# Kernel optimization log

Hardware: AMD Instinct MI355X
Metric: run time of the kernel (lower is better)

The kernel has to match this reference:

```python
import jax, jax.numpy as jnp
import numpy as np

N = 50000      # nodes
E = 600000     # edges
G = 256        # graphs in batch
HID = 128      # gcn hidden = gcn in = gcn out
EDIM = 16      # edge feature dim
EH = 64        # edge mlp hidden
NL = 4         # gcn layers
MIN_ = 200     # mol feature dim
MH = 256       # mlp hidden
MOUT = 128     # mlp out
PH = 512       # predictor hidden
PIN = HID + MOUT


def setup_inputs() -> dict:
    key = jax.random.key(0)
    ks = jax.random.split(key, 32)
    f = lambda k, s: jax.random.normal(k, s, dtype=jnp.float32)
    p = lambda k, s: 0.05 * jax.random.normal(k, s, dtype=jnp.float32)
    return {
        "x": f(ks[0], (N, HID)),
        "edge_index": jax.random.randint(ks[1], (2, E), 0, N),
        "edge_attr": f(ks[2], (E, EDIM)),
        "batch_index": jnp.sort(jax.random.randint(ks[3], (N,), 0, G)),
        "mol_features": f(ks[4], (G, MIN_)),
        # PDNConv params (stacked over NL layers)
        "conv_lin_W": p(ks[5], (NL, HID, HID)),
        "conv_mW1": p(ks[6], (NL, EDIM, EH)),
        "conv_mb1": p(ks[7], (NL, EH)),
        "conv_mW2": p(ks[8], (NL, EH)),
        "conv_mb2": p(ks[9], (NL,)),
        "conv_bias": p(ks[10], (NL, HID)),
        # dense Linear after each conv
        "gcn_W": p(ks[11], (NL, HID, HID)),
        "gcn_b": p(ks[12], (NL, HID)),
        # mol-feature MLP (n_mlp_layers=3 -> 4 linears)
        "mlp_W0": p(ks[13], (MIN_, MH)), "mlp_b0": p(ks[14], (MH,)),
        "mlp_W1": p(ks[15], (MH, MH)),   "mlp_b1": p(ks[16], (MH,)),
        "mlp_W2": p(ks[17], (MH, MH)),   "mlp_b2": p(ks[18], (MH,)),
        "mlp_W3": p(ks[19], (MH, MOUT)), "mlp_b3": p(ks[20], (MOUT,)),
        # predictor
        "pred_W0": p(ks[21], (PIN, PH)), "pred_b0": p(ks[22], (PH,)),
        "pred_W1": p(ks[23], (PH, PH)),  "pred_b1": p(ks[24], (PH,)),
        "out_W": p(ks[25], (PH, 1)),     "out_b": p(ks[26], (1,)),
    }


def _pdn_conv(h, row, col, edge_attr, lin_W, mW1, mb1, mW2, mb2, bias):
    # edge MLP -> sigmoid gate (PyG PDNConv)
    w = jax.nn.sigmoid(jnp.maximum(edge_attr @ mW1 + mb1, 0.0) @ mW2 + mb2)  # [E]
    # gcn_norm with self loops (fill weight 1.0)
    loop = jnp.arange(N)
    r = jnp.concatenate([row, loop])
    c = jnp.concatenate([col, loop])
    w_all = jnp.concatenate([w, jnp.ones((N,), h.dtype)])
    deg = jax.ops.segment_sum(w_all, c, num_segments=N)
    dinv = jnp.where(deg > 0, jax.lax.rsqrt(deg), 0.0)
    norm = dinv[r] * w_all * dinv[c]                                          # [E+N]
    hl = h @ lin_W                                                            # [N,HID]
    out = jax.ops.segment_sum(norm[:, None] * hl[r], c, num_segments=N)
    return out + bias


def reference(x, edge_index, edge_attr, batch_index, mol_features,
              conv_lin_W, conv_mW1, conv_mb1, conv_mW2, conv_mb2, conv_bias,
              gcn_W, gcn_b,
              mlp_W0, mlp_b0, mlp_W1, mlp_b1, mlp_W2, mlp_b2, mlp_W3, mlp_b3,
              pred_W0, pred_b0, pred_W1, pred_b1, out_W, out_b):
    row, col = edge_index[0], edge_index[1]
    relu = lambda v: jnp.maximum(v, 0.0)

    # GCN stack: PDNConv -> relu(Linear), x NL
    h1 = x
    for i in range(NL):
        h1 = _pdn_conv(h1, row, col, edge_attr, conv_lin_W[i], conv_mW1[i],
                       conv_mb1[i], conv_mW2[i], conv_mb2[i], conv_bias[i])
        h1 = relu(h1 @ gcn_W[i] + gcn_b[i])
    # global mean pool over graphs
    sums = jax.ops.segment_sum(h1, batch_index, num_segments=G)
    cnts = jax.ops.segment_sum(jnp.ones((N,), h1.dtype), batch_index, num_segments=G)
    h1 = sums / jnp.maximum(cnts, 1.0)[:, None]                               # [G,HID]

    # molecular-feature MLP
    h2 = relu(mol_features @ mlp_W0 + mlp_b0)
    h2 = relu(h2 @ mlp_W1 + mlp_b1)
    h2 = relu(h2 @ mlp_W2 + mlp_b2)
    h2 = relu(h2 @ mlp_W3 + mlp_b3)                                           # [G,MOUT]

    h = jnp.concatenate([h1, h2], axis=1)                                     # [G,PIN]
    h = relu(h @ pred_W0 + pred_b0)
    h = relu(h @ pred_W1 + pred_b1)
    return h @ out_W + out_b                                                  # [G,1]
```

## Files before the change

### kernel.cpp

```cpp
#include <hip/hip_runtime.h>
#include <hip/hip_bf16.h>


#define NN 50000
#define EE 600000
#define GG 256
#define HID 128
#define EDIM 16
#define EHID 64
#define NL 4
#define MIN_F 200
#define MH 256
#define MOUT 128
#define PH 512
#define PIN 256
#define SCAN_B 196
#define PCH 8

typedef __hip_bfloat16 bf16;
typedef __attribute__((ext_vector_type(8))) short bf16x8;
typedef __attribute__((ext_vector_type(4))) float f32x4;

__device__ __forceinline__ float bfl(unsigned u) { return __uint_as_float(u << 16); }
__device__ __forceinline__ float bfh(unsigned u) { return __uint_as_float(u & 0xffff0000u); }
__device__ __forceinline__ float b2f(bf16 x) { return __bfloat162float(x); }
__device__ __forceinline__ float ldf(const void* p, long i, bool bf) {
  return bf ? __bfloat162float(((const bf16*)p)[i]) : ((const float*)p)[i];
}
__device__ __forceinline__ unsigned short f2bf_bits(float v) {
  bf16 h = __float2bfloat16(v);
  return *reinterpret_cast<unsigned short*>(&h);
}

__global__ void probe_kernel(const unsigned short* __restrict__ xs, int* flag) {
  if (threadIdx.x == 0 && blockIdx.x == 0) {
    int sane = 0;
    for (int i = 0; i < 128; i++) {
      unsigned e = (xs[i] >> 7) & 0xFF;
      if (e >= 96 && e <= 159) sane++;
    }
    *flag = (sane >= 112) ? 1 : 0;
  }
}

__global__ __launch_bounds__(256) void cvt_to_bf16(const void* __restrict__ in,
                                                   unsigned short* __restrict__ outp,
                                                   int n8, const int* __restrict__ flag) {
  bool bf = *flag != 0;
  int i = blockIdx.x * 256 + threadIdx.x;
  if (i >= n8) return;
  if (bf) {
    reinterpret_cast<uint4*>(outp)[i] = reinterpret_cast<const uint4*>(in)[i];
  } else {
    const float4* p = reinterpret_cast<const float4*>(in) + (size_t)i * 2;
    float4 v0 = p[0], v1 = p[1];
    ushort4 a, b;
    a.x = f2bf_bits(v0.x); a.y = f2bf_bits(v0.y);
    a.z = f2bf_bits(v0.z); a.w = f2bf_bits(v0.w);
    b.x = f2bf_bits(v1.x); b.y = f2bf_bits(v1.y);
    b.z = f2bf_bits(v1.z); b.w = f2bf_bits(v1.w);
    reinterpret_cast<ushort4*>(outp)[i * 2] = a;
    reinterpret_cast<ushort4*>(outp)[i * 2 + 1] = b;
  }
}

__global__ __launch_bounds__(256) void cvt_molf(const void* __restrict__ in,
                                                float* __restrict__ outp,
                                                const int* __restrict__ flag) {
  bool bf = *flag != 0;
  int i = blockIdx.x * 256 + threadIdx.x;
  if (i >= GG * 50) return;
  int row = i / 50, c4 = (i % 50) * 4;
  float4 v;
  if (bf) {
    const unsigned short* p = (const unsigned short*)in + (size_t)row * MIN_F + c4;
    uint2 u = *reinterpret_cast<const uint2*>(p);
    v.x = bfl(u.x); v.y = bfh(u.x); v.z = bfl(u.y); v.w = bfh(u.y);
  } else {
    v = *reinterpret_cast<const float4*>((const float*)in + (size_t)row * MIN_F + c4);
  }
  *reinterpret_cast<float4*>(&outp[(size_t)row * 256 + c4]) = v;
}

__global__ __launch_bounds__(256) void prep_fused_w(const void* __restrict__ lin_W,
                                                    const void* __restrict__ gW,
                                                    unsigned short* __restrict__ Wt,
                                                    const int* __restrict__ flag) {
  bool bf = *flag != 0;
  int idx = blockIdx.x * 256 + threadIdx.x;
  if (idx >= 4 * 16384) return;
  int l = idx >> 14;
  int rem = idx & 16383;
  int n = rem >> 7, k = rem & 127;
  float s = 0.f;
  long lb = (long)l * 16384;
  for (int m = 0; m < 128; m++)
    s += ldf(lin_W, lb + (long)k * 128 + m, bf) * ldf(gW, lb + (long)m * 128 + n, bf);
  Wt[idx] = f2bf_bits(s);
}

__global__ __launch_bounds__(128) void prep_fused_b(const void* __restrict__ cbias,
                                                    const void* __restrict__ gW,
                                                    const void* __restrict__ gb,
                                                    float* __restrict__ bprime,
                                                    const int* __restrict__ flag) {
  bool bf = *flag != 0;
  int idx = blockIdx.x * 128 + threadIdx.x;
  if (idx >= NL * HID) return;
  int l = idx >> 7, n = idx & 127;
  float s = ldf(gb, idx, bf);
  long lb = (long)l * 16384;
  for (int k = 0; k < 128; k++)
    s += ldf(cbias, (long)l * 128 + k, bf) * ldf(gW, lb + (long)k * 128 + n, bf);
  bprime[idx] = s;
}

__global__ __launch_bounds__(256) void prep_edge_w(const void* __restrict__ mW1,
                                                   const void* __restrict__ mb1,
                                                   unsigned short* __restrict__ W1t,
                                                   const int* __restrict__ flag) {
  bool bf = *flag != 0;
  int idx = blockIdx.x * 256 + threadIdx.x;
  if (idx >= 256 * 32) return;
  int col = idx >> 5, k = idx & 31;
  float v = 0.f;
  if (k < EDIM) v = ldf(mW1, (long)(col >> 6) * (EDIM * EHID) + (long)k * EHID + (col & 63), bf);
  else if (k == EDIM) v = ldf(mb1, col, bf);
  W1t[idx] = f2bf_bits(v);
}

__global__ __launch_bounds__(256) void prep_tail(
    const void* __restrict__ mlpW0, const void* __restrict__ mlpW1,
    const void* __restrict__ mlpW2, const void* __restrict__ mlpW3,
    const void* __restrict__ predW0, const void* __restrict__ predW1,
    unsigned short* __restrict__ T, const int* __restrict__ flag) {
  bool bf = *flag != 0;
  int idx = blockIdx.x * 256 + threadIdx.x;
  const void* src; int N, Kp, Ksrc, off;
  if      (idx < 65536)  { src = mlpW0;  N = 256; Kp = 256; Ksrc = 200; off = 0; }
  else if (idx < 131072) { src = mlpW1;  N = 256; Kp = 256; Ksrc = 256; off = 65536; }
  else if (idx < 196608) { src = mlpW2;  N = 256; Kp = 256; Ksrc = 256; off = 131072; }
  else if (idx < 229376) { src = mlpW3;  N = 128; Kp = 256; Ksrc = 256; off = 196608; }
  else if (idx < 360448) { src = predW0; N = 512; Kp = 256; Ksrc = 256; off = 229376; }
  else if (idx < 622592) { src = predW1; N = 512; Kp = 512; Ksrc = 512; off = 360448; }
  else return;
  int rem = idx - off;
  int n = rem / Kp, k = rem % Kp;
  float v = (k < Ksrc) ? ldf(src, (long)k * N + n, bf) : 0.f;
  T[idx] = f2bf_bits(v);
}

__global__ __launch_bounds__(256) void count_kernel(const int* __restrict__ ei,
                                                    int* __restrict__ cnt) {
  int e = blockIdx.x * 256 + threadIdx.x;
  if (e >= EE) return;
  int c = ei[EE + e];
  c = min(max(c, 0), NN - 1);
  atomicAdd(&cnt[c], 1);
}

__global__ __launch_bounds__(256) void scan_phase1(const int* __restrict__ cnt,
                                                   int* __restrict__ bsum) {
  __shared__ int red[256];
  int tid = threadIdx.x;
  int i = blockIdx.x * 256 + tid;
  red[tid] = (i < NN) ? cnt[i] : 0;
  __syncthreads();
  for (int off = 128; off > 0; off >>= 1) {
    if (tid < off) red[tid] += red[tid + off];
    __syncthreads();
  }
  if (tid == 0) bsum[blockIdx.x] = red[0];
}

__global__ __launch_bounds__(256) void scan_phase2(int* __restrict__ bsum,
                                                   int* __restrict__ offs) {
  __shared__ int buf[256];
  int tid = threadIdx.x;
  int v = (tid < SCAN_B) ? bsum[tid] : 0;
  buf[tid] = v;
  __syncthreads();
  for (int off = 1; off < 256; off <<= 1) {
    int t = (tid >= off) ? buf[tid - off] : 0;
    __syncthreads();
    buf[tid] += t;
    __syncthreads();
  }
  if (tid < SCAN_B) bsum[tid] = buf[tid] - v;
  if (tid == 255) offs[NN] = buf[255];
}

__global__ __launch_bounds__(256) void scan_phase3(const int* __restrict__ cnt,
                                                   const int* __restrict__ bsum,
                                                   int* __restrict__ offs) {
  __shared__ int buf[256];
  int tid = threadIdx.x;
  int i = blockIdx.x * 256 + tid;
  int v = (i < NN) ? cnt[i] : 0;
  buf[tid] = v;
  __syncthreads();
  for (int off = 1; off < 256; off <<= 1) {
    int t = (tid >= off) ? buf[tid - off] : 0;
    __syncthreads();
    buf[tid] += t;
    __syncthreads();
  }
  if (i < NN) offs[i] = bsum[blockIdx.x] + buf[tid] - v;
}

__global__ __launch_bounds__(256) void fill_kernel(const int* __restrict__ ei,
                                                   const int* __restrict__ offs,
                                                   int* __restrict__ cursor,
                                                   int2* __restrict__ csr_se) {
  int e = blockIdx.x * 256 + threadIdx.x;
  if (e >= EE) return;
  int c = ei[EE + e];
  c = min(max(c, 0), NN - 1);
  int pos = offs[c] + atomicAdd(&cursor[c], 1);
  pos = min(max(pos, 0), EE - 1);
  csr_se[pos] = make_int2(ei[e], e);
}

__global__ __launch_bounds__(256) void edge_mlp_mfma(
    const void* __restrict__ eattr, const unsigned short* __restrict__ W1t,
    const void* __restrict__ mW2, const void* __restrict__ mb2,
    float* __restrict__ w_all4, const int* __restrict__ flag) {
  bool bf = *flag != 0;
  int tid = threadIdx.x;
  int wave = tid >> 6, lane = tid & 63;
  int l15 = lane & 15, quad = lane >> 4;

  bf16x8 bfrag[16];
#pragma unroll
  for (int t = 0; t < 16; t++)
    bfrag[t] = *reinterpret_cast<const bf16x8*>(&W1t[(t * 16 + l15) * 32 + quad * 8]);

  float w2v[16];
#pragma unroll
  for (int t = 0; t < 16; t++) w2v[t] = ldf(mW2, t * 16 + l15, bf);
  float b2v0 = ldf(mb2, 0, bf), b2v1 = ldf(mb2, 1, bf);
  float b2v2 = ldf(mb2, 2, bf), b2v3 = ldf(mb2, 3, bf);
  float b2 = b2v0;
  b2 = (l15 == 1) ? b2v1 : b2;
  b2 = (l15 == 2) ? b2v2 : b2;
  b2 = (l15 == 3) ? b2v3 : b2;
  bool o1 = (l15 & 1) != 0;
  bool o2 = (l15 & 2) != 0;

  int ebase = blockIdx.x * 512 + wave * 128;
#pragma unroll 1
  for (int f = 0; f < 8; f++) {
    int fbase = ebase + f * 16;
    if (fbase < EE) {
      long erow = fbase + l15;
      bf16x8 a = (bf16x8){0, 0, 0, 0, 0, 0, 0, 0};
      if (quad < 2) {
        if (bf) {
          uint4 v = *reinterpret_cast<const uint4*>((const bf16*)eattr + erow * EDIM + quad * 8);
          a = *reinterpret_cast<bf16x8*>(&v);
        } else {
          const float4* p =
              reinterpret_cast<const float4*>((const float*)eattr + erow * EDIM + quad * 8);
          float4 v0 = p[0], v1 = p[1];
          a[0] = (short)f2bf_bits(v0.x); a[1] = (short)f2bf_bits(v0.y);
          a[2] = (short)f2bf_bits(v0.z); a[3] = (short)f2bf_bits(v0.w);
          a[4] = (short)f2bf_bits(v1.x); a[5] = (short)f2bf_bits(v1.y);
          a[6] = (short)f2bf_bits(v1.z); a[7] = (short)f2bf_bits(v1.w);
        }
      }
      if (quad == 2) a[0] = (short)0x3F80;
      float s00 = 0.f, s01 = 0.f, s02 = 0.f, s03 = 0.f;
      float s10 = 0.f, s11 = 0.f, s12 = 0.f, s13 = 0.f;
      float s20 = 0.f, s21 = 0.f, s22 = 0.f, s23 = 0.f;
      float s30 = 0.f, s31 = 0.f, s32 = 0.f, s33 = 0.f;
#define DO_T(T, S0, S1, S2, S3)                                               \
  {                                                                           \
    f32x4 acc = __builtin_amdgcn_mfma_f32_16x16x32_bf16(                      \
        a, bfrag[T], (f32x4){0.f, 0.f, 0.f, 0.f}, 0, 0, 0);                   \
    S0 += fmaxf(acc.x, 0.f) * w2v[T];                                         \
    S1 += fmaxf(acc.y, 0.f) * w2v[T];                                         \
    S2 += fmaxf(acc.z, 0.f) * w2v[T];                                         \
    S3 += fmaxf(acc.w, 0.f) * w2v[T];                                         \
  }
      DO_T(0,  s00, s01, s02, s03) DO_T(1,  s00, s01, s02, s03)
      DO_T(2,  s00, s01, s02, s03) DO_T(3,  s00, s01, s02, s03)
      DO_T(4,  s10, s11, s12, s13) DO_T(5,  s10, s11, s12, s13)
      DO_T(6,  s10, s11, s12, s13) DO_T(7,  s10, s11, s12, s13)
      DO_T(8,  s20, s21, s22, s23) DO_T(9,  s20, s21, s22, s23)
      DO_T(10, s20, s21, s22, s23) DO_T(11, s20, s21, s22, s23)
      DO_T(12, s30, s31, s32, s33) DO_T(13, s30, s31, s32, s33)
      DO_T(14, s30, s31, s32, s33) DO_T(15, s30, s31, s32, s33)
#undef DO_T
#define RS_STEP1(AR, S0R, S1R) \
  float AR = (o1 ? S1R : S0R) + __shfl_xor(o1 ? S0R : S1R, 1);
      RS_STEP1(a0, s00, s10)
      RS_STEP1(a1, s01, s11)
      RS_STEP1(a2, s02, s12)
      RS_STEP1(a3, s03, s13)
      RS_STEP1(bb0, s20, s30)
      RS_STEP1(bb1, s21, s31)
      RS_STEP1(bb2, s22, s32)
      RS_STEP1(bb3, s23, s33)
#undef RS_STEP1
      float c0 = (o2 ? bb0 : a0) + __shfl_xor(o2 ? a0 : bb0, 2);
      float c1 = (o2 ? bb1 : a1) + __shfl_xor(o2 ? a1 : bb1, 2);
      float c2 = (o2 ? bb2 : a2) + __shfl_xor(o2 ? a2 : bb2, 2);
      float c3 = (o2 ? bb3 : a3) + __shfl_xor(o2 ? a3 : bb3, 2);
      c0 += __shfl_xor(c0, 4); c1 += __shfl_xor(c1, 4);
      c2 += __shfl_xor(c2, 4); c3 += __shfl_xor(c3, 4);
      c0 += __shfl_xor(c0, 8); c1 += __shfl_xor(c1, 8);
      c2 += __shfl_xor(c2, 8); c3 += __shfl_xor(c3, 8);
      if (l15 < NL) {
        float g0 = 1.f / (1.f + __expf(-(c0 + b2)));
        float g1 = 1.f / (1.f + __expf(-(c1 + b2)));
        float g2 = 1.f / (1.f + __expf(-(c2 + b2)));
        float g3 = 1.f / (1.f + __expf(-(c3 + b2)));
        w_all4[(size_t)(fbase + quad * 4 + 0) * 4 + l15] = g0;
        w_all4[(size_t)(fbase + quad * 4 + 1) * 4 + l15] = g1;
        w_all4[(size_t)(fbase + quad * 4 + 2) * 4 + l15] = g2;
        w_all4[(size_t)(fbase + quad * 4 + 3) * 4 + l15] = g3;
      }
    }
  }
}

__global__ __launch_bounds__(256) void csr_gather(const int2* __restrict__ csr_se,
                                                  const float* __restrict__ w_all4,
                                                  float* __restrict__ csr_val) {
  int k = blockIdx.x * 256 + threadIdx.x;
  if (k >= EE) return;
  int eid = csr_se[k].y;
  eid = min(max(eid, 0), EE - 1);
  float4 w = reinterpret_cast<const float4*>(w_all4)[eid];
  csr_val[k] = w.x;
  csr_val[(size_t)EE + k] = w.y;
  csr_val[2 * (size_t)EE + k] = w.z;
  csr_val[3 * (size_t)EE + k] = w.w;
}

__global__ __launch_bounds__(256) void deg_kernel(const int* __restrict__ offs,
                                                  const float* __restrict__ csr_val,
                                                  float* __restrict__ dinv4) {
  int n = blockIdx.x * 256 + threadIdx.x;
  if (n >= NN) return;
  int s = offs[n], e = offs[n + 1];
  float d0 = 1.f, d1 = 1.f, d2 = 1.f, d3 = 1.f;
  for (int k = s; k < e; k++) {
    d0 += csr_val[k];
    d1 += csr_val[EE + k];
    d2 += csr_val[2 * (size_t)EE + k];
    d3 += csr_val[3 * (size_t)EE + k];
  }
  float4 o;
  o.x = rsqrtf(d0); o.y = rsqrtf(d1); o.z = rsqrtf(d2); o.w = rsqrtf(d3);
  reinterpret_cast<float4*>(dinv4)[n] = o;
}

__global__ __launch_bounds__(256) void csr_scale_kernel(const int2* __restrict__ csr_se,
                                                        const float* __restrict__ dinv4,
                                                        float* __restrict__ csr_val) {
  int k = blockIdx.x * 256 + threadIdx.x;
  if (k >= EE) return;
  int s = csr_se[k].x;
  s = min(max(s, 0), NN - 1);
  float4 d = reinterpret_cast<const float4*>(dinv4)[s];
  csr_val[k] *= d.x;
  csr_val[(size_t)EE + k] *= d.y;
  csr_val[2 * (size_t)EE + k] *= d.z;
  csr_val[3 * (size_t)EE + k] *= d.w;
}

__global__ __launch_bounds__(256) void gemm_nodes_bf16(
    const unsigned short* __restrict__ A16, const unsigned short* __restrict__ Wt,
    const float* __restrict__ bias, unsigned short* __restrict__ out16,
    int relu) {
  __shared__ alignas(16) unsigned short sA[64 * 136];
  __shared__ alignas(16) unsigned short sW[128 * 136];
  int tid = threadIdx.x;
  int rbase = blockIdx.x * 64;

#pragma unroll
  for (int p = 0; p < 8; p++) {
    int idx8 = p * 256 + tid;
    int n = idx8 >> 4, kc = idx8 & 15;
    uint4 v = reinterpret_cast<const uint4*>(Wt)[idx8];
    *reinterpret_cast<uint4*>(&sW[n * 136 + kc * 8]) = v;
  }
#pragma unroll
  for (int p = 0; p < 4; p++) {
    int idx8 = p * 256 + tid;
    int m = idx8 >> 4, kc = idx8 & 15;
    int row = rbase + m;
    uint4 v = make_uint4(0u, 0u, 0u, 0u);
    if (row < NN)
      v = *reinterpret_cast<const uint4*>(&A16[(size_t)row * HID + kc * 8]);
    *reinterpret_cast<uint4*>(&sA[m * 136 + kc * 8]) = v;
  }
  __syncthreads();

  int wave = tid >> 6, lane = tid & 63;
  int l15 = lane & 15, quad = lane >> 4;
  int mstrip = wave * 16;

  f32x4 acc[8];
#pragma unroll
  for (int t = 0; t < 8; t++) acc[t] = (f32x4){0.f, 0.f, 0.f, 0.f};

#pragma unroll
  for (int ks = 0; ks < 4; ks++) {
    int k0 = ks * 32 + quad * 8;
    bf16x8 a = *reinterpret_cast<const bf16x8*>(&sA[(mstrip + l15) * 136 + k0]);
#pragma unroll
    for (int t = 0; t < 8; t++) {
      bf16x8 b = *reinterpret_cast<const bf16x8*>(&sW[(t * 16 + l15) * 136 + k0]);
      acc[t] = __builtin_amdgcn_mfma_f32_16x16x32_bf16(a, b, acc[t], 0, 0, 0);
    }
  }

#pragma unroll
  for (int t = 0; t < 8; t++) {
    int n = t * 16 + l15;
    float bv = bias ? bias[n] : 0.f;
#pragma unroll
    for (int r = 0; r < 4; r++) {
      int row = rbase + mstrip + quad * 4 + r;
      if (row < NN) {
        float o = acc[t][r] + bv;
        if (relu) o = fmaxf(o, 0.f);
        out16[(size_t)row * HID + n] = f2bf_bits(o);
      }
    }
  }
}

__global__ __launch_bounds__(256) void gemm_tail_mfma(
    const float* __restrict__ A, int lda, const unsigned short* __restrict__ Wt,
    int Kp, const void* __restrict__ bias, float* __restrict__ outp, int ldo,
    int relu, const int* __restrict__ flag) {
  __shared__ alignas(16) unsigned short sA[64 * 264];
  __shared__ alignas(16) unsigned short sW[64 * 264];
  int tid = threadIdx.x;
  int rbase = blockIdx.x * 64;
  int nbase = blockIdx.y * 64;
  int wave = tid >> 6, lane = tid & 63;
  int l15 = lane & 15, quad = lane >> 4;
  int mstrip = wave * 16;

  f32x4 acc[4];
#pragma unroll
  for (int t = 0; t < 4; t++) acc[t] = (f32x4){0.f, 0.f, 0.f, 0.f};

  for (int kc = 0; kc < Kp; kc += 256) {
#pragma unroll 4
    for (int p = 0; p < 16; p++) {
      int idx = p * 1024 + tid * 4;
      int m = idx >> 8, k = idx & 255;
      float4 v = *reinterpret_cast<const float4*>(&A[(size_t)(rbase + m) * lda + kc + k]);
      ushort4 b;
      b.x = f2bf_bits(v.x); b.y = f2bf_bits(v.y);
      b.z = f2bf_bits(v.z); b.w = f2bf_bits(v.w);
      *reinterpret_cast<ushort4*>(&sA[m * 264 + k]) = b;
    }
#pragma unroll 4
    for (int p = 0; p < 8; p++) {
      int idx8 = p * 256 + tid;
      int n = idx8 >> 5, kk = (idx8 & 31) * 8;
      uint4 v = *reinterpret_cast<const uint4*>(&Wt[(size_t)(nbase + n) * Kp + kc + kk]);
      *reinterpret_cast<uint4*>(&sW[n * 264 + kk]) = v;
    }
    __syncthreads();
#pragma unroll
    for (int ks = 0; ks < 8; ks++) {
      int k0 = ks * 32 + quad * 8;
      bf16x8 a = *reinterpret_cast<const bf16x8*>(&sA[(mstrip + l15) * 264 + k0]);
#pragma unroll
      for (int nt = 0; nt < 4; nt++) {
        bf16x8 b = *reinterpret_cast<const bf16x8*>(&sW[(nt * 16 + l15) * 264 + k0]);
        acc[nt] = __builtin_amdgcn_mfma_f32_16x16x32_bf16(a, b, acc[nt], 0, 0, 0);
      }
    }
    __syncthreads();
  }

  bool bf = *flag != 0;
#pragma unroll
  for (int nt = 0; nt < 4; nt++) {
    int col = nbase + nt * 16 + l15;
    float bv = ldf(bias, col, bf);
#pragma unroll
    for (int r = 0; r < 4; r++) {
      int row = rbase + mstrip + quad * 4 + r;
      float o = acc[nt][r] + bv;
      if (relu) o = fmaxf(o, 0.f);
      outp[(size_t)row * ldo + col] = o;
    }
  }
}

__global__ __launch_bounds__(64) void aggregate_kernel(
    const unsigned short* __restrict__ h16, const int* __restrict__ offs,
    const int2* __restrict__ csr_se, const float* __restrict__ csr_val,
    const float* __restrict__ dinv4, int layer,
    unsigned short* __restrict__ out16) {
  int n = blockIdx.x;
  int lane = threadIdx.x;
  int grp = lane >> 4;
  int c16 = lane & 15;
  __shared__ int s_src[64];
  __shared__ float s_val[64];
  int start = offs[n], end = offs[n + 1];
  float a0 = 0.f, a1 = 0.f, a2 = 0.f, a3 = 0.f;
  float a4 = 0.f, a5 = 0.f, a6 = 0.f, a7 = 0.f;
  for (int base = start; base < end; base += 64) {
    int k = base + lane;
    if (k < end) {
      s_src[lane] = min(max(csr_se[k].x, 0), NN - 1);
      s_val[lane] = csr_val[k];
    }
    __syncthreads();
    int m = min(64, end - base);
    for (int j = grp; j < m; j += 4) {
      float v = s_val[j];
      uint4 u = *reinterpret_cast<const uint4*>(&h16[(size_t)s_src[j] * HID + c16 * 8]);
      a0 = fmaf(v, bfl(u.x), a0); a1 = fmaf(v, bfh(u.x), a1);
      a2 = fmaf(v, bfl(u.y), a2); a3 = fmaf(v, bfh(u.y), a3);
      a4 = fmaf(v, bfl(u.z), a4); a5 = fmaf(v, bfh(u.z), a5);
      a6 = fmaf(v, bfl(u.w), a6); a7 = fmaf(v, bfh(u.w), a7);
    }
    __syncthreads();
  }
  a0 += __shfl_xor(a0, 16); a1 += __shfl_xor(a1, 16);
  a2 += __shfl_xor(a2, 16); a3 += __shfl_xor(a3, 16);
  a4 += __shfl_xor(a4, 16); a5 += __shfl_xor(a5, 16);
  a6 += __shfl_xor(a6, 16); a7 += __shfl_xor(a7, 16);
  a0 += __shfl_xor(a0, 32); a1 += __shfl_xor(a1, 32);
  a2 += __shfl_xor(a2, 32); a3 += __shfl_xor(a3, 32);
  a4 += __shfl_xor(a4, 32); a5 += __shfl_xor(a5, 32);
  a6 += __shfl_xor(a6, 32); a7 += __shfl_xor(a7, 32);
  if (grp == 0) {
    float dn = dinv4[(size_t)n * 4 + layer];
    float dn2 = dn * dn;
    uint4 su = *reinterpret_cast<const uint4*>(&h16[(size_t)n * HID + c16 * 8]);
    ushort4 o0, o1v;
    o0.x  = f2bf_bits(dn * a0 + dn2 * bfl(su.x));
    o0.y  = f2bf_bits(dn * a1 + dn2 * bfh(su.x));
    o0.z  = f2bf_bits(dn * a2 + dn2 * bfl(su.y));
    o0.w  = f2bf_bits(dn * a3 + dn2 * bfh(su.y));
    o1v.x = f2bf_bits(dn * a4 + dn2 * bfl(su.z));
    o1v.y = f2bf_bits(dn * a5 + dn2 * bfh(su.z));
    o1v.z = f2bf_bits(dn * a6 + dn2 * bfl(su.w));
    o1v.w = f2bf_bits(dn * a7 + dn2 * bfh(su.w));
    *reinterpret_cast<ushort4*>(&out16[(size_t)n * HID + c16 * 8]) = o0;
    *reinterpret_cast<ushort4*>(&out16[(size_t)n * HID + c16 * 8 + 4]) = o1v;
  }
}

__global__ __launch_bounds__(128) void pool_partial(const unsigned short* __restrict__ h16,
                                                    const int* __restrict__ batch,
                                                    float* __restrict__ part) {
  int g = blockIdx.x, chunk = blockIdx.y, c = threadIdx.x;
  int lo = 0, hi = NN;
  while (lo < hi) { int mid = (lo + hi) >> 1; if (batch[mid] < g) lo = mid + 1; else hi = mid; }
  int start = lo;
  hi = NN;
  while (lo < hi) { int mid = (lo + hi) >> 1; if (batch[mid] < g + 1) lo = mid + 1; else hi = mid; }
  int end = lo;
  int len = end - start;
  int per = (len + PCH - 1) / PCH;
  int s = start + chunk * per;
  int e = min(s + per, end);
  float sum = 0.f;
  for (int n = s; n < e; n++) sum += bfl((unsigned)h16[(size_t)n * HID + c]);
  part[((size_t)g * PCH + chunk) * HID + c] = sum;
}

__global__ __launch_bounds__(128) void pool_combine(const float* __restrict__ part,
                                                    const int* __restrict__ batch,
                                                    float* __restrict__ cat) {
  int g = blockIdx.x, c = threadIdx.x;
  int lo = 0, hi = NN;
  while (lo < hi) { int mid = (lo + hi) >> 1; if (batch[mid] < g) lo = mid + 1; else hi = mid; }
  int start = lo;
  hi = NN;
  while (lo < hi) { int mid = (lo + hi) >> 1; if (batch[mid] < g + 1) lo = mid + 1; else hi = mid; }
  int end = lo;
  float s = 0.f;
#pragma unroll
  for (int k = 0; k < PCH; k++) s += part[((size_t)g * PCH + k) * HID + c];
  float cntf = (float)(end - start);
  cat[(size_t)g * PIN + c] = s / fmaxf(cntf, 1.f);
}

__global__ __launch_bounds__(64) void final_kernel(const float* __restrict__ A,
                                                   const void* __restrict__ W,
                                                   const void* __restrict__ b,
                                                   void* __restrict__ outp,
                                                   const int* __restrict__ flag) {
  bool bf = *flag != 0;
  int g = blockIdx.x, lane = threadIdx.x;
  float s = 0.f;
  for (int k = lane; k < PH; k += 64) s = fmaf(A[(size_t)g * PH + k], ldf(W, k, bf), s);
#pragma unroll
  for (int off = 32; off > 0; off >>= 1) s += __shfl_down(s, off);
  if (lane == 0) {
    float r = s + ldf(b, 0, bf);
    if (bf) ((bf16*)outp)[g] = __float2bfloat16(r);
    else    ((float*)outp)[g] = r;
  }
}

extern "C" void kernel_launch(void* const* d_in, const int* in_sizes, int n_in,
                              void* d_out, int out_size, void* d_ws, size_t ws_size,
                              hipStream_t stream) {
  const void* x      = d_in[0];
  const int*  ei     = (const int*)d_in[1];
  const void* eattr  = d_in[2];
  const int*  batch  = (const int*)d_in[3];
  const void* molf   = d_in[4];
  const void* lin_W  = d_in[5];
  const void* mW1    = d_in[6];
  const void* mb1    = d_in[7];
  const void* mW2    = d_in[8];
  const void* mb2    = d_in[9];
  const void* cbias  = d_in[10];
  const void* gW     = d_in[11];
  const void* gb     = d_in[12];
  const void* mlpW0  = d_in[13];
  const void* mlpb0  = d_in[14];
  const void* mlpW1  = d_in[15];
  const void* mlpb1  = d_in[16];
  const void* mlpW2  = d_in[17];
  const void* mlpb2  = d_in[18];
  const void* mlpW3  = d_in[19];
  const void* mlpb3  = d_in[20];
  const void* predW0 = d_in[21];
  const void* predb0 = d_in[22];
  const void* predW1 = d_in[23];
  const void* predb1 = d_in[24];
  const void* outW   = d_in[25];
  const void* outb   = d_in[26];

  char* base = (char*)d_ws;
  size_t off = 0;
  auto alloc = [&](size_t bytes) -> char* {
    char* p = base + off;
    off = (off + bytes + 255) & ~(size_t)255;
    return p;
  };
  unsigned short* h16  = (unsigned short*)alloc((size_t)NN * HID * 2);
  unsigned short* t16  = (unsigned short*)alloc((size_t)NN * HID * 2);
  float* dinv4    = (float*)alloc((size_t)NN * 4 * 4);
  int*   cnt      = (int*)alloc((size_t)NN * 4);
  int*   offs     = (int*)alloc((size_t)(NN + 1) * 4);
  int*   cursor   = (int*)alloc((size_t)NN * 4);
  int*   bsum     = (int*)alloc((size_t)256 * 4);
  int2*  csr_se   = (int2*)alloc((size_t)EE * 8);
  float* csr_val  = (float*)alloc((size_t)NL * EE * 4);
  float* w_all4   = (float*)alloc((size_t)EE * 4 * 4);
  unsigned short* Wt    = (unsigned short*)alloc((size_t)NL * HID * HID * 2);
  float* bprime   = (float*)alloc((size_t)NL * HID * 4);
  unsigned short* tailW = (unsigned short*)alloc((size_t)622592 * 2);
  unsigned short* edgeW = (unsigned short*)alloc((size_t)256 * 32 * 2);
  int*   flag     = (int*)alloc(256);
  float* part     = (float*)alloc((size_t)GG * PCH * HID * 4);
  float* molf32   = (float*)alloc((size_t)GG * 256 * 4);
  float* m0       = (float*)alloc((size_t)GG * MH * 4);
  float* m1       = (float*)alloc((size_t)GG * MH * 4);
  float* cat      = (float*)alloc((size_t)GG * PIN * 4);
  float* p0       = (float*)alloc((size_t)GG * PH * 4);
  float* p1       = (float*)alloc((size_t)GG * PH * 4);

  hipMemsetAsync(cnt, 0, (size_t)NN * 4, stream);
  hipMemsetAsync(cursor, 0, (size_t)NN * 4, stream);
  hipMemsetAsync(molf32, 0, (size_t)GG * 256 * 4, stream);

  probe_kernel<<<1, 64, 0, stream>>>((const unsigned short*)x, flag);

  prep_fused_w<<<256, 256, 0, stream>>>(lin_W, gW, Wt, flag);
  prep_fused_b<<<NL, 128, 0, stream>>>(cbias, gW, gb, bprime, flag);
  prep_tail<<<(622592 + 255) / 256, 256, 0, stream>>>(mlpW0, mlpW1, mlpW2, mlpW3,
                                                      predW0, predW1, tailW, flag);
  prep_edge_w<<<32, 256, 0, stream>>>(mW1, mb1, edgeW, flag);

  {
    int n8 = NN * HID / 8;
    cvt_to_bf16<<<(n8 + 255) / 256, 256, 0, stream>>>(x, h16, n8, flag);
  }
  edge_mlp_mfma<<<(EE + 511) / 512, 256, 0, stream>>>(eattr, edgeW, mW2, mb2,
                                                      w_all4, flag);
  count_kernel<<<(EE + 255) / 256, 256, 0, stream>>>(ei, cnt);
  scan_phase1<<<SCAN_B, 256, 0, stream>>>(cnt, bsum);
  scan_phase2<<<1, 256, 0, stream>>>(bsum, offs);
  scan_phase3<<<SCAN_B, 256, 0, stream>>>(cnt, bsum, offs);
  fill_kernel<<<(EE + 255) / 256, 256, 0, stream>>>(ei, offs, cursor, csr_se);
  csr_gather<<<(EE + 255) / 256, 256, 0, stream>>>(csr_se, w_all4, csr_val);
  deg_kernel<<<(NN + 255) / 256, 256, 0, stream>>>(offs, csr_val, dinv4);
  csr_scale_kernel<<<(EE + 255) / 256, 256, 0, stream>>>(csr_se, dinv4, csr_val);

  const int gemm_blocks = (NN + 63) / 64;
  for (int l = 0; l < NL; l++) {
    aggregate_kernel<<<NN, 64, 0, stream>>>(h16, offs, csr_se,
                                            csr_val + (size_t)l * EE, dinv4, l, t16);
    gemm_nodes_bf16<<<gemm_blocks, 256, 0, stream>>>(
        t16, Wt + (size_t)l * HID * HID, bprime + (size_t)l * HID, h16, 1);
  }

  pool_partial<<<dim3(GG, PCH), 128, 0, stream>>>(h16, batch, part);
  pool_combine<<<GG, 128, 0, stream>>>(part, batch, cat);

  cvt_molf<<<(GG * 50 + 255) / 256, 256, 0, stream>>>(molf, molf32, flag);
  gemm_tail_mfma<<<dim3(4, 4), 256, 0, stream>>>(molf32, 256, tailW + 0,      256, mlpb0, m0, 256, 1, flag);
  gemm_tail_mfma<<<dim3(4, 4), 256, 0, stream>>>(m0,     256, tailW + 65536,  256, mlpb1, m1, 256, 1, flag);
  gemm_tail_mfma<<<dim3(4, 4), 256, 0, stream>>>(m1,     256, tailW + 131072, 256, mlpb2, m0, 256, 1, flag);
  gemm_tail_mfma<<<dim3(4, 2), 256, 0, stream>>>(m0,     256, tailW + 196608, 256, mlpb3, cat + MOUT, 256, 1, flag);

  gemm_tail_mfma<<<dim3(4, 8), 256, 0, stream>>>(cat, 256, tailW + 229376, 256, predb0, p0, 512, 1, flag);
  gemm_tail_mfma<<<dim3(4, 8), 256, 0, stream>>>(p0,  512, tailW + 360448, 512, predb1, p1, 512, 1, flag);
  final_kernel<<<GG, 64, 0, stream>>>(p1, outW, outb, d_out, flag);
}
```

Measured before the change: 578.7 us.

## Fuse neighbor aggregation into node GEMM and merge CSR weight preprocessing kernels

Each GCN layer's separate aggregate kernel and node GEMM become a single kernel. Each 64-node block gathers neighbor features with wave shuffles, writes the normalized aggregate straight into shared memory, and then runs the MFMA GEMM on it. This removes the intermediate bf16 activation round-trip through global memory and one launch per layer. The CSR weight gather, degree and scale kernels are also collapsed into two kernels that read the edge gates directly. The risk is parallelism: each wave now walks 16 nodes one after another, so far fewer waves are available to hide the latency of the irregular gathers.

```diff
diff --git a/kernel.cpp b/kernel.cpp
--- a/kernel.cpp
+++ b/kernel.cpp
@@ -324,60 +324,53 @@
   }
 }
 
-__global__ __launch_bounds__(256) void csr_gather(const int2* __restrict__ csr_se,
+__global__ __launch_bounds__(256) void deg_kernel(const int* __restrict__ offs,
+                                                  const int2* __restrict__ csr_se,
                                                   const float* __restrict__ w_all4,
-                                                  float* __restrict__ csr_val) {
-  int k = blockIdx.x * 256 + threadIdx.x;
-  if (k >= EE) return;
-  int eid = csr_se[k].y;
-  eid = min(max(eid, 0), EE - 1);
-  float4 w = reinterpret_cast<const float4*>(w_all4)[eid];
-  csr_val[k] = w.x;
-  csr_val[(size_t)EE + k] = w.y;
-  csr_val[2 * (size_t)EE + k] = w.z;
-  csr_val[3 * (size_t)EE + k] = w.w;
-}
-
-__global__ __launch_bounds__(256) void deg_kernel(const int* __restrict__ offs,
-                                                  const float* __restrict__ csr_val,
                                                   float* __restrict__ dinv4) {
   int n = blockIdx.x * 256 + threadIdx.x;
   if (n >= NN) return;
   int s = offs[n], e = offs[n + 1];
   float d0 = 1.f, d1 = 1.f, d2 = 1.f, d3 = 1.f;
   for (int k = s; k < e; k++) {
-    d0 += csr_val[k];
-    d1 += csr_val[EE + k];
-    d2 += csr_val[2 * (size_t)EE + k];
-    d3 += csr_val[3 * (size_t)EE + k];
+    int eid = min(max(csr_se[k].y, 0), EE - 1);
+    float4 w = reinterpret_cast<const float4*>(w_all4)[eid];
+    d0 += w.x; d1 += w.y; d2 += w.z; d3 += w.w;
   }
   float4 o;
   o.x = rsqrtf(d0); o.y = rsqrtf(d1); o.z = rsqrtf(d2); o.w = rsqrtf(d3);
   reinterpret_cast<float4*>(dinv4)[n] = o;
 }
 
-__global__ __launch_bounds__(256) void csr_scale_kernel(const int2* __restrict__ csr_se,
-                                                        const float* __restrict__ dinv4,
-                                                        float* __restrict__ csr_val) {
+__global__ __launch_bounds__(256) void csr_build_val(const int2* __restrict__ csr_se,
+                                                     const float* __restrict__ w_all4,
+                                                     const float* __restrict__ dinv4,
+                                                     float* __restrict__ csr_val) {
   int k = blockIdx.x * 256 + threadIdx.x;
   if (k >= EE) return;
-  int s = csr_se[k].x;
-  s = min(max(s, 0), NN - 1);
+  int2 se = csr_se[k];
+  int s = min(max(se.x, 0), NN - 1);
+  int eid = min(max(se.y, 0), EE - 1);
+  float4 w = reinterpret_cast<const float4*>(w_all4)[eid];
   float4 d = reinterpret_cast<const float4*>(dinv4)[s];
-  csr_val[k] *= d.x;
-  csr_val[(size_t)EE + k] *= d.y;
-  csr_val[2 * (size_t)EE + k] *= d.z;
-  csr_val[3 * (size_t)EE + k] *= d.w;
-}
-
-__global__ __launch_bounds__(256) void gemm_nodes_bf16(
-    const unsigned short* __restrict__ A16, const unsigned short* __restrict__ Wt,
-    const float* __restrict__ bias, unsigned short* __restrict__ out16,
-    int relu) {
+  csr_val[k] = w.x * d.x;
+  csr_val[(size_t)EE + k] = w.y * d.y;
+  csr_val[2 * (size_t)EE + k] = w.z * d.z;
+  csr_val[3 * (size_t)EE + k] = w.w * d.w;
+}
+
+__global__ __launch_bounds__(256) void agg_gemm_fused(
+    const unsigned short* __restrict__ h16, const int* __restrict__ offs,
+    const int2* __restrict__ csr_se, const float* __restrict__ csr_val,
+    const float* __restrict__ dinv4, int layer,
+    const unsigned short* __restrict__ Wt, const float* __restrict__ bias,
+    unsigned short* __restrict__ out16) {
   __shared__ alignas(16) unsigned short sA[64 * 136];
   __shared__ alignas(16) unsigned short sW[128 * 136];
   int tid = threadIdx.x;
   int rbase = blockIdx.x * 64;
+  int wave = tid >> 6, lane = tid & 63;
+  int grp = lane >> 4, c16 = lane & 15;
 
 #pragma unroll
   for (int p = 0; p < 8; p++) {
@@ -386,26 +379,68 @@
     uint4 v = reinterpret_cast<const uint4*>(Wt)[idx8];
     *reinterpret_cast<uint4*>(&sW[n * 136 + kc * 8]) = v;
   }
-#pragma unroll
-  for (int p = 0; p < 4; p++) {
-    int idx8 = p * 256 + tid;
-    int m = idx8 >> 4, kc = idx8 & 15;
-    int row = rbase + m;
-    uint4 v = make_uint4(0u, 0u, 0u, 0u);
-    if (row < NN)
-      v = *reinterpret_cast<const uint4*>(&A16[(size_t)row * HID + kc * 8]);
-    *reinterpret_cast<uint4*>(&sA[m * 136 + kc * 8]) = v;
+
+#pragma unroll 1
+  for (int i = 0; i < 16; i++) {
+    int m_local = wave * 16 + i;
+    int node = rbase + m_local;
+    if (node < NN) {
+      int start = offs[node], end = offs[node + 1];
+      float a0 = 0.f, a1 = 0.f, a2 = 0.f, a3 = 0.f;
+      float a4 = 0.f, a5 = 0.f, a6 = 0.f, a7 = 0.f;
+      for (int base = start; base < end; base += 64) {
+        int k = base + lane;
+        int srcR = 0;
+        float valR = 0.f;
+        if (k < end) {
+          int2 se = csr_se[k];
+          srcR = min(max(se.x, 0), NN - 1);
+          valR = csr_val[k];
+        }
+        int m = min(64, end - base);
+        for (int j = grp; j < m; j += 4) {
+          float v = __shfl(valR, j);
+          int s = __shfl(srcR, j);
+          uint4 u = *reinterpret_cast<const uint4*>(&h16[(size_t)s * HID + c16 * 8]);
+          a0 = fmaf(v, bfl(u.x), a0); a1 = fmaf(v, bfh(u.x), a1);
+          a2 = fmaf(v, bfl(u.y), a2); a3 = fmaf(v, bfh(u.y), a3);
+          a4 = fmaf(v, bfl(u.z), a4); a5 = fmaf(v, bfh(u.z), a5);
+          a6 = fmaf(v, bfl(u.w), a6); a7 = fmaf(v, bfh(u.w), a7);
+        }
+      }
+      a0 += __shfl_xor(a0, 16); a1 += __shfl_xor(a1, 16);
+      a2 += __shfl_xor(a2, 16); a3 += __shfl_xor(a3, 16);
+      a4 += __shfl_xor(a4, 16); a5 += __shfl_xor(a5, 16);
+      a6 += __shfl_xor(a6, 16); a7 += __shfl_xor(a7, 16);
+      a0 += __shfl_xor(a0, 32); a1 += __shfl_xor(a1, 32);
+      a2 += __shfl_xor(a2, 32); a3 += __shfl_xor(a3, 32);
+      a4 += __shfl_xor(a4, 32); a5 += __shfl_xor(a5, 32);
+      a6 += __shfl_xor(a6, 32); a7 += __shfl_xor(a7, 32);
+      if (grp == 0) {
+        float dn = dinv4[(size_t)node * 4 + layer];
+        float dn2 = dn * dn;
+        uint4 su = *reinterpret_cast<const uint4*>(&h16[(size_t)node * HID + c16 * 8]);
+        ushort4 o0, o1v;
+        o0.x  = f2bf_bits(dn * a0 + dn2 * bfl(su.x));
+        o0.y  = f2bf_bits(dn * a1 + dn2 * bfh(su.x));
+        o0.z  = f2bf_bits(dn * a2 + dn2 * bfl(su.y));
+        o0.w  = f2bf_bits(dn * a3 + dn2 * bfh(su.y));
+        o1v.x = f2bf_bits(dn * a4 + dn2 * bfl(su.z));
+        o1v.y = f2bf_bits(dn * a5 + dn2 * bfh(su.z));
+        o1v.z = f2bf_bits(dn * a6 + dn2 * bfl(su.w));
+        o1v.w = f2bf_bits(dn * a7 + dn2 * bfh(su.w));
+        *reinterpret_cast<ushort4*>(&sA[m_local * 136 + c16 * 8]) = o0;
+        *reinterpret_cast<ushort4*>(&sA[m_local * 136 + c16 * 8 + 4]) = o1v;
+      }
+    }
   }
   __syncthreads();
 
-  int wave = tid >> 6, lane = tid & 63;
   int l15 = lane & 15, quad = lane >> 4;
   int mstrip = wave * 16;
-
   f32x4 acc[8];
 #pragma unroll
   for (int t = 0; t < 8; t++) acc[t] = (f32x4){0.f, 0.f, 0.f, 0.f};
-
 #pragma unroll
   for (int ks = 0; ks < 4; ks++) {
     int k0 = ks * 32 + quad * 8;
@@ -416,17 +451,15 @@
       acc[t] = __builtin_amdgcn_mfma_f32_16x16x32_bf16(a, b, acc[t], 0, 0, 0);
     }
   }
-
 #pragma unroll
   for (int t = 0; t < 8; t++) {
     int n = t * 16 + l15;
-    float bv = bias ? bias[n] : 0.f;
+    float bv = bias[n];
 #pragma unroll
     for (int r = 0; r < 4; r++) {
       int row = rbase + mstrip + quad * 4 + r;
       if (row < NN) {
-        float o = acc[t][r] + bv;
-        if (relu) o = fmaxf(o, 0.f);
+        float o = fmaxf(acc[t][r] + bv, 0.f);
         out16[(size_t)row * HID + n] = f2bf_bits(o);
       }
     }
@@ -494,64 +527,6 @@
       if (relu) o = fmaxf(o, 0.f);
       outp[(size_t)row * ldo + col] = o;
     }
-  }
-}
-
-__global__ __launch_bounds__(64) void aggregate_kernel(
-    const unsigned short* __restrict__ h16, const int* __restrict__ offs,
-    const int2* __restrict__ csr_se, const float* __restrict__ csr_val,
-    const float* __restrict__ dinv4, int layer,
-    unsigned short* __restrict__ out16) {
-  int n = blockIdx.x;
-  int lane = threadIdx.x;
-  int grp = lane >> 4;
-  int c16 = lane & 15;
-  __shared__ int s_src[64];
-  __shared__ float s_val[64];
-  int start = offs[n], end = offs[n + 1];
-  float a0 = 0.f, a1 = 0.f, a2 = 0.f, a3 = 0.f;
-  float a4 = 0.f, a5 = 0.f, a6 = 0.f, a7 = 0.f;
-  for (int base = start; base < end; base += 64) {
-    int k = base + lane;
-    if (k < end) {
-      s_src[lane] = min(max(csr_se[k].x, 0), NN - 1);
-      s_val[lane] = csr_val[k];
-    }
-    __syncthreads();
-    int m = min(64, end - base);
-    for (int j = grp; j < m; j += 4) {
-      float v = s_val[j];
-      uint4 u = *reinterpret_cast<const uint4*>(&h16[(size_t)s_src[j] * HID + c16 * 8]);
-      a0 = fmaf(v, bfl(u.x), a0); a1 = fmaf(v, bfh(u.x), a1);
-      a2 = fmaf(v, bfl(u.y), a2); a3 = fmaf(v, bfh(u.y), a3);
-      a4 = fmaf(v, bfl(u.z), a4); a5 = fmaf(v, bfh(u.z), a5);
-      a6 = fmaf(v, bfl(u.w), a6); a7 = fmaf(v, bfh(u.w), a7);
-    }
-    __syncthreads();
-  }
-  a0 += __shfl_xor(a0, 16); a1 += __shfl_xor(a1, 16);
-  a2 += __shfl_xor(a2, 16); a3 += __shfl_xor(a3, 16);
-  a4 += __shfl_xor(a4, 16); a5 += __shfl_xor(a5, 16);
-  a6 += __shfl_xor(a6, 16); a7 += __shfl_xor(a7, 16);
-  a0 += __shfl_xor(a0, 32); a1 += __shfl_xor(a1, 32);
-  a2 += __shfl_xor(a2, 32); a3 += __shfl_xor(a3, 32);
-  a4 += __shfl_xor(a4, 32); a5 += __shfl_xor(a5, 32);
-  a6 += __shfl_xor(a6, 32); a7 += __shfl_xor(a7, 32);
-  if (grp == 0) {
-    float dn = dinv4[(size_t)n * 4 + layer];
-    float dn2 = dn * dn;
-    uint4 su = *reinterpret_cast<const uint4*>(&h16[(size_t)n * HID + c16 * 8]);
-    ushort4 o0, o1v;
-    o0.x  = f2bf_bits(dn * a0 + dn2 * bfl(su.x));
-    o0.y  = f2bf_bits(dn * a1 + dn2 * bfh(su.x));
-    o0.z  = f2bf_bits(dn * a2 + dn2 * bfl(su.y));
-    o0.w  = f2bf_bits(dn * a3 + dn2 * bfh(su.y));
-    o1v.x = f2bf_bits(dn * a4 + dn2 * bfl(su.z));
-    o1v.y = f2bf_bits(dn * a5 + dn2 * bfh(su.z));
-    o1v.z = f2bf_bits(dn * a6 + dn2 * bfl(su.w));
-    o1v.w = f2bf_bits(dn * a7 + dn2 * bfh(su.w));
-    *reinterpret_cast<ushort4*>(&out16[(size_t)n * HID + c16 * 8]) = o0;
-    *reinterpret_cast<ushort4*>(&out16[(size_t)n * HID + c16 * 8 + 4]) = o1v;
   }
 }
 
@@ -693,19 +668,20 @@
   scan_phase2<<<1, 256, 0, stream>>>(bsum, offs);
   scan_phase3<<<SCAN_B, 256, 0, stream>>>(cnt, bsum, offs);
   fill_kernel<<<(EE + 255) / 256, 256, 0, stream>>>(ei, offs, cursor, csr_se);
-  csr_gather<<<(EE + 255) / 256, 256, 0, stream>>>(csr_se, w_all4, csr_val);
-  deg_kernel<<<(NN + 255) / 256, 256, 0, stream>>>(offs, csr_val, dinv4);
-  csr_scale_kernel<<<(EE + 255) / 256, 256, 0, stream>>>(csr_se, dinv4, csr_val);
+  deg_kernel<<<(NN + 255) / 256, 256, 0, stream>>>(offs, csr_se, w_all4, dinv4);
+  csr_build_val<<<(EE + 255) / 256, 256, 0, stream>>>(csr_se, w_all4, dinv4, csr_val);
 
   const int gemm_blocks = (NN + 63) / 64;
+  unsigned short* hcur = h16;
+  unsigned short* hnxt = t16;
   for (int l = 0; l < NL; l++) {
-    aggregate_kernel<<<NN, 64, 0, stream>>>(h16, offs, csr_se,
-                                            csr_val + (size_t)l * EE, dinv4, l, t16);
-    gemm_nodes_bf16<<<gemm_blocks, 256, 0, stream>>>(
-        t16, Wt + (size_t)l * HID * HID, bprime + (size_t)l * HID, h16, 1);
-  }
-
-  pool_partial<<<dim3(GG, PCH), 128, 0, stream>>>(h16, batch, part);
+    agg_gemm_fused<<<gemm_blocks, 256, 0, stream>>>(
+        hcur, offs, csr_se, csr_val + (size_t)l * EE, dinv4, l,
+        Wt + (size_t)l * HID * HID, bprime + (size_t)l * HID, hnxt);
+    unsigned short* tmp = hcur; hcur = hnxt; hnxt = tmp;
+  }
+
+  pool_partial<<<dim3(GG, PCH), 128, 0, stream>>>(hcur, batch, part);
   pool_combine<<<GG, 128, 0, stream>>>(part, batch, cat);
 
   cvt_molf<<<(GG * 50 + 255) / 256, 256, 0, stream>>>(molf, molf32, flag);
```

Measured after the change: 748.2 us. 29.3% more time.
